# Performance work log

Hardware: AMD Instinct MI355X
Metric: run time of the kernel (lower is better)

Reference implementation:

```python
import jax, jax.numpy as jnp
import numpy as np

N, E, NG, G = 40000, 400000, 64, 512
IN, GP, SP, EP, EA = 4, 3, 3, 6, 4
HID, HEADS, L = 192, 4, 3
DH, FFN = HID // HEADS, 2 * HID


def _ln(x, g, b, eps=1e-5):
    m = x.mean(-1, keepdims=True)
    v = ((x - m) ** 2).mean(-1, keepdims=True)
    return (x - m) * jax.lax.rsqrt(v + eps) * g + b


def _forward(x, edge_attr, group_probs, splitter_probs, endpoint_preds, params,
             edge_index, batch, group_ptr, time_group_ids):
    (W_in, b_in, Wq, Wk, Wv, We, Wo, bo, ln1_g, ln1_b,
     W_ff1, b_ff1, W_ff2, b_ff2, ln2_g, ln2_b,
     W_e1, b_e1, W_e2, b_e2, W_e3, b_e3) = params
    n = x.shape[0]
    src, dst = edge_index[0], edge_index[1]
    # expand per-group predictions to per-node via group ids
    gids = jnp.clip(group_ptr[batch] + time_group_ids, 0, group_probs.shape[0] - 1)
    feat = jnp.concatenate([x, group_probs[gids], splitter_probs, endpoint_preds[gids]], axis=1)
    h = feat @ W_in + b_in  # [N, HID]
    scale = np.float32(1.0 / np.sqrt(DH))
    for l in range(L):  # graph transformer blocks (attention restricted to edges)
        q = (h @ Wq[l]).reshape(n, HEADS, DH)
        k = (h @ Wk[l]).reshape(n, HEADS, DH)
        v = (h @ Wv[l]).reshape(n, HEADS, DH)
        e = (edge_attr @ We[l]).reshape(-1, HEADS, DH)  # [E, H, DH]
        ke = k[src] + e
        ve = v[src] + e
        logit = jnp.einsum('ehd,ehd->eh', q[dst], ke) * scale  # [E, H]
        m = jax.ops.segment_max(logit, dst, num_segments=n)
        m = jnp.where(jnp.isfinite(m), m, 0.0)  # guard nodes with no incoming edges
        a = jnp.exp(logit - m[dst])
        den = jax.ops.segment_sum(a, dst, num_segments=n)
        a = a / (den[dst] + 1e-16)  # per-destination softmax over incoming edges
        msg = jax.ops.segment_sum(a[:, :, None] * ve, dst, num_segments=n).reshape(n, HID)
        h = _ln(h + msg @ Wo[l] + bo[l], ln1_g[l], ln1_b[l])
        ff = jax.nn.relu(h @ W_ff1[l] + b_ff1[l]) @ W_ff2[l] + b_ff2[l]
        h = _ln(h + ff, ln2_g[l], ln2_b[l])
    # edge head: gather src/dst embeddings + edge_attr, concat, MLP -> per-edge logit
    pair = jnp.concatenate([h[src], h[dst], edge_attr], axis=1)  # [E, 2*HID+EA]
    z = jax.nn.relu(pair @ W_e1 + b_e1)
    z = jax.nn.relu(z @ W_e2 + b_e2)
    return z @ W_e3 + b_e3  # [E, 1]


def setup_inputs() -> dict:
    key = jax.random.key(0)
    ks = list(jax.random.split(key, 32))
    it = iter(ks)

    def g(shape, scale=0.05):
        return jax.random.normal(next(it), shape, jnp.float32) * scale

    inp = {
        'x': jax.random.normal(next(it), (N, IN), jnp.float32),
        'edge_index': jax.random.randint(next(it), (2, E), 0, N),
        'edge_attr': jax.random.normal(next(it), (E, EA), jnp.float32),
        'batch': jnp.sort(jax.random.randint(next(it), (N,), 0, NG)),
        'group_ptr': jnp.arange(NG + 1),
        'time_group_ids': jax.random.randint(next(it), (N,), 0, 8),
        'group_probs': jax.random.normal(next(it), (G, GP), jnp.float32),
        'splitter_probs': jax.random.normal(next(it), (N, SP), jnp.float32),
        'endpoint_preds': jax.random.normal(next(it), (G, EP), jnp.float32),
        'W_in': g((IN + GP + SP + EP, HID)), 'b_in': jnp.zeros((HID,), jnp.float32),
        'Wq': g((L, HID, HID)), 'Wk': g((L, HID, HID)), 'Wv': g((L, HID, HID)),
        'We': g((L, EA, HID)), 'Wo': g((L, HID, HID)), 'bo': jnp.zeros((L, HID), jnp.float32),
        'ln1_g': jnp.ones((L, HID), jnp.float32), 'ln1_b': jnp.zeros((L, HID), jnp.float32),
        'W_ff1': g((L, HID, FFN)), 'b_ff1': jnp.zeros((L, FFN), jnp.float32),
        'W_ff2': g((L, FFN, HID)), 'b_ff2': jnp.zeros((L, HID), jnp.float32),
        'ln2_g': jnp.ones((L, HID), jnp.float32), 'ln2_b': jnp.zeros((L, HID), jnp.float32),
        'W_e1': g((2 * HID + EA, HID)), 'b_e1': jnp.zeros((HID,), jnp.float32),
        'W_e2': g((HID, HID // 2)), 'b_e2': jnp.zeros((HID // 2,), jnp.float32),
        'W_e3': g((HID // 2, 1)), 'b_e3': jnp.zeros((1,), jnp.float32),
    }
    return inp


def reference(x, edge_index, edge_attr, batch, group_ptr, time_group_ids,
              group_probs, splitter_probs, endpoint_preds,
              W_in, b_in, Wq, Wk, Wv, We, Wo, bo, ln1_g, ln1_b,
              W_ff1, b_ff1, W_ff2, b_ff2, ln2_g, ln2_b,
              W_e1, b_e1, W_e2, b_e2, W_e3, b_e3):
    params = (W_in, b_in, Wq, Wk, Wv, We, Wo, bo, ln1_g, ln1_b,
              W_ff1, b_ff1, W_ff2, b_ff2, ln2_g, ln2_b,
              W_e1, b_e1, W_e2, b_e2, W_e3, b_e3)
    return _forward(x, edge_attr, group_probs, splitter_probs, endpoint_preds, params,
                    edge_index, batch, group_ptr, time_group_ids)
```

## Files before the change

### kernel.cpp

```cpp
#include <hip/hip_runtime.h>
#include <hip/hip_bf16.h>
#include <math.h>

#define N_NODES 40000
#define N_EDGES 400000
#define GCLIP 511

using short8  = __attribute__((ext_vector_type(8))) short;
using ushort8 = __attribute__((ext_vector_type(8))) unsigned short;
using floatx4 = __attribute__((ext_vector_type(4))) float;

__device__ __forceinline__ void split_bf16(float v, unsigned short& hi, unsigned short& lo) {
    __hip_bfloat16 h = __float2bfloat16(v);
    float r = v - __bfloat162float(h);
    __hip_bfloat16 l = __float2bfloat16(r);
    hi = *(unsigned short*)&h;
    lo = *(unsigned short*)&l;
}
__device__ __forceinline__ unsigned short f2bf(float f) {
    __hip_bfloat16 h = __float2bfloat16(f);
    return *(unsigned short*)&h;
}
__device__ __forceinline__ float bf2f(unsigned short u) {
    __hip_bfloat16 h = *(__hip_bfloat16*)&u;
    return __bfloat162float(h);
}
__device__ __forceinline__ floatx4 mfma16(short8 a, short8 b, floatx4 c) {
    return __builtin_amdgcn_mfma_f32_16x16x32_bf16(a, b, c, 0, 0, 0);
}

__global__ void count_kernel(const int* __restrict__ dst, int* __restrict__ cnt, int E) {
    int e = blockIdx.x * 256 + threadIdx.x;
    if (e < E) atomicAdd(&cnt[dst[e]], 1);
}

__global__ void scan1_kernel(const int* __restrict__ cnt, int* __restrict__ rowp,
                             int* __restrict__ bsum, int n) {
    __shared__ int wsum[16];
    __shared__ int woff[16];
    int tid = threadIdx.x, wave = tid >> 6, lane = tid & 63;
    int i = blockIdx.x * 1024 + tid;
    int v = (i < n) ? cnt[i] : 0;
    int x = v;
    for (int off = 1; off < 64; off <<= 1) {
        int t = __shfl_up(x, off);
        if (lane >= off) x += t;
    }
    if (lane == 63) wsum[wave] = x;
    __syncthreads();
    if (wave == 0 && lane < 16) {
        int s = wsum[lane];
        for (int off = 1; off < 16; off <<= 1) {
            int t = __shfl_up(s, off);
            if (lane >= off) s += t;
        }
        woff[lane] = s;
    }
    __syncthreads();
    int incl = x + ((wave == 0) ? 0 : woff[wave - 1]);
    if (i < n) rowp[i] = incl - v;
    if (tid == 1023) bsum[blockIdx.x] = incl;
}

__global__ void scan2_kernel(const int* __restrict__ bsum, int* __restrict__ boffs,
                             int* __restrict__ rowp, int nb, int n) {
    int lane = threadIdx.x;
    int v = (lane < nb) ? bsum[lane] : 0;
    int x = v;
    for (int off = 1; off < 64; off <<= 1) {
        int t = __shfl_up(x, off);
        if (lane >= off) x += t;
    }
    if (lane < nb) boffs[lane] = x - v;
    if (lane == nb - 1) rowp[n] = x;
}

__global__ void scan3_kernel(int* __restrict__ rowp, int* __restrict__ curs,
                             const int* __restrict__ boffs, int n) {
    int i = blockIdx.x * 1024 + threadIdx.x;
    if (i < n) {
        int v = rowp[i] + boffs[blockIdx.x];
        rowp[i] = v;
        curs[i] = v;
    }
}

__global__ void scatter_kernel(const int* __restrict__ src, const int* __restrict__ dst,
                               int* __restrict__ cursor, int2* __restrict__ csr2, int E) {
    int e = blockIdx.x * 256 + threadIdx.x;
    if (e < E) {
        int pos = atomicAdd(&cursor[dst[e]], 1);
        csr2[pos] = make_int2(src[e], e);
    }
}

__global__ void feat_kernel(const float* __restrict__ x, const int* __restrict__ batch,
                            const int* __restrict__ gptr, const int* __restrict__ tgid,
                            const float* __restrict__ gp, const float* __restrict__ sp,
                            const float* __restrict__ ep,
                            unsigned short* __restrict__ fhi, unsigned short* __restrict__ flo,
                            int n) {
    int idx = blockIdx.x * 256 + threadIdx.x;
    if (idx >= n * 32) return;
    int node = idx >> 5, c = idx & 31;
    float v = 0.f;
    if (c < 4) {
        v = x[node * 4 + c];
    } else if (c < 7) {
        int gid = gptr[batch[node]] + tgid[node];
        gid = min(max(gid, 0), GCLIP);
        v = gp[gid * 3 + (c - 4)];
    } else if (c < 10) {
        v = sp[node * 3 + (c - 7)];
    } else if (c < 16) {
        int gid = gptr[batch[node]] + tgid[node];
        gid = min(max(gid, 0), GCLIP);
        v = ep[gid * 6 + (c - 10)];
    }
    unsigned short hi, lo;
    split_bf16(v, hi, lo);
    fhi[idx] = hi;
    flo[idx] = lo;
}

#define WOFF_WIN 0
#define WOFF_QKV 6144
#define WOFF_WO  337920
#define WOFF_WF1 448512
#define WOFF_WF2 669696
#define WOFF_HSD 890880
#define WOFF_WE2 964608
#define WTOT     983040

__global__ void prep_kernel(const float* __restrict__ W_in, const float* __restrict__ Wq,
                            const float* __restrict__ Wk, const float* __restrict__ Wv,
                            const float* __restrict__ Wo, const float* __restrict__ Wf1,
                            const float* __restrict__ Wf2, const float* __restrict__ We1,
                            const float* __restrict__ We2, unsigned short* __restrict__ wb) {
    int idx = blockIdx.x * 256 + threadIdx.x;
    if (idx >= WTOT) return;
    float val;
    if (idx < WOFF_QKV) {
        int n = idx / 32, k = idx % 32;
        val = (k < 16) ? W_in[k * 192 + n] : 0.f;
    } else if (idx < WOFF_WO) {
        int r = idx - WOFF_QKV; int l = r / 110592; r %= 110592;
        int n = r / 192, k = r % 192;
        const float* s = (n < 192) ? Wq : (n < 384 ? Wk : Wv);
        val = s[l * 36864 + k * 192 + (n % 192)];
        if (n < 192) val *= 0.14433756729740643f;
    } else if (idx < WOFF_WF1) {
        int r = idx - WOFF_WO; int l = r / 36864; r %= 36864;
        int n = r / 192, k = r % 192;
        val = Wo[l * 36864 + k * 192 + n];
    } else if (idx < WOFF_WF2) {
        int r = idx - WOFF_WF1; int l = r / 73728; r %= 73728;
        int n = r / 192, k = r % 192;
        val = Wf1[l * 73728 + k * 384 + n];
    } else if (idx < WOFF_HSD) {
        int r = idx - WOFF_WF2; int l = r / 73728; r %= 73728;
        int n = r / 384, k = r % 384;
        val = Wf2[l * 73728 + k * 192 + n];
    } else if (idx < WOFF_WE2) {
        int r = idx - WOFF_HSD;
        int n = r / 192, k = r % 192;
        val = (n < 192) ? We1[k * 192 + n] : We1[(192 + k) * 192 + (n - 192)];
    } else {
        int r = idx - WOFF_WE2;
        int n = r / 192, k = r % 192;
        val = We2[k * 96 + n];
    }
    wb[idx] = f2bf(val);
}


template <int EPI, int DUAL, int BN, int KCH, int TERMS, int MT>
__global__ __launch_bounds__(256, 4)
void mfma_gemm(const unsigned short* __restrict__ Ahi, const unsigned short* __restrict__ Alo,
               int M, int Ka,
               const unsigned short* __restrict__ B, const float* __restrict__ bias,
               const unsigned short* __restrict__ Rhi, const unsigned short* __restrict__ Rlo,
               const float* __restrict__ lng, const float* __restrict__ lnb,
               unsigned short* __restrict__ Chi, unsigned short* __restrict__ Clo, int ldc) {
    constexpr int NT = BN / 16;
    constexpr int JB = KCH / 8;
    constexpr int SBLK = ((JB + 7) / 8) * 8;
    __shared__ __align__(16) unsigned short sB[BN * SBLK * 8];
    const int tid = threadIdx.x;
    const int wave = tid >> 6, lane = tid & 63;
    const int quad = lane >> 4, l16 = lane & 15;
    const int rbase = blockIdx.x * 64 * MT;
    const int cbase = blockIdx.y * BN;

    floatx4 acc[MT][NT];
#pragma unroll
    for (int mt = 0; mt < MT; ++mt)
#pragma unroll
        for (int nt = 0; nt < NT; ++nt) acc[mt][nt] = (floatx4)0.0f;

    const unsigned short* pah[MT];
    const unsigned short* pal[MT];
#pragma unroll
    for (int mt = 0; mt < MT; ++mt) {
        int r = min(rbase + wave * 16 * MT + mt * 16 + l16, M - 1);
        pah[mt] = Ahi + (size_t)r * Ka + quad * 8;
        pal[mt] = Alo + (size_t)r * Ka + quad * 8;
    }

    for (int kb = 0; kb < Ka; kb += KCH) {
        if (kb) __syncthreads();
        for (int i = tid; i < BN * JB; i += 256) {
            int n = i % BN, j = i / BN;
            *(uint4*)&sB[(n * SBLK + (j ^ (n & 7))) * 8] =
                *(const uint4*)(B + (size_t)(cbase + n) * Ka + kb + j * 8);
        }
        __syncthreads();
        short8 ch[MT], cl[MT];
#pragma unroll
        for (int mt = 0; mt < MT; ++mt) {
            ch[mt] = *(const short8*)(pah[mt] + kb);
            if (TERMS == 2) cl[mt] = *(const short8*)(pal[mt] + kb);
        }
#pragma unroll
        for (int kc = 0; kc < KCH; kc += 32) {
            short8 nh[MT], nl[MT];
#pragma unroll
            for (int mt = 0; mt < MT; ++mt) { nh[mt] = ch[mt]; nl[mt] = ch[mt]; }
            if (kc + 32 < KCH) {
#pragma unroll
                for (int mt = 0; mt < MT; ++mt) {
                    nh[mt] = *(const short8*)(pah[mt] + kb + kc + 32);
                    if (TERMS == 2) nl[mt] = *(const short8*)(pal[mt] + kb + kc + 32);
                }
            }
            const int jbase = kc / 8;
#pragma unroll
            for (int nt = 0; nt < NT; ++nt) {
                int jj = (jbase + quad) ^ (l16 & 7);
                short8 b = *(const short8*)&sB[((nt * 16 + l16) * SBLK + jj) * 8];
#pragma unroll
                for (int mt = 0; mt < MT; ++mt) {
                    acc[mt][nt] = mfma16(ch[mt], b, acc[mt][nt]);
                    if (TERMS == 2) acc[mt][nt] = mfma16(cl[mt], b, acc[mt][nt]);
                }
            }
#pragma unroll
            for (int mt = 0; mt < MT; ++mt) {
                ch[mt] = nh[mt];
                if (TERMS == 2) cl[mt] = nl[mt];
            }
        }
    }

    float bb[NT], gg[NT], be[NT];
#pragma unroll
    for (int nt = 0; nt < NT; ++nt) {
        int colg = cbase + nt * 16 + l16;
        bb[nt] = bias ? bias[colg] : 0.f;
        if (EPI == 2) { gg[nt] = lng[colg]; be[nt] = lnb[colg]; }
    }
#pragma unroll
    for (int mt = 0; mt < MT; ++mt) {
#pragma unroll
        for (int reg = 0; reg < 4; ++reg) {
            int row = rbase + wave * 16 * MT + mt * 16 + quad * 4 + reg;
            if (EPI == 2) {
                int rr = min(row, M - 1);
                float v[NT], s = 0.f, q = 0.f;
#pragma unroll
                for (int nt = 0; nt < NT; ++nt) {
                    size_t off = (size_t)rr * 192 + nt * 16 + l16;
                    float resid = bf2f(Rhi[off]);
                    if (DUAL) resid += bf2f(Rlo[off]);
                    v[nt] = acc[mt][nt][reg] + bb[nt] + resid;
                    s += v[nt]; q += v[nt] * v[nt];
                }
#pragma unroll
                for (int off = 1; off < 16; off <<= 1) {
                    s += __shfl_xor(s, off);
                    q += __shfl_xor(q, off);
                }
                float mean = s * (1.f / 192.f);
                float var = q * (1.f / 192.f) - mean * mean;
                float rs = rsqrtf(var + 1e-5f);
                if (row < M) {
#pragma unroll
                    for (int nt = 0; nt < NT; ++nt) {
                        float r = (v[nt] - mean) * rs * gg[nt] + be[nt];
                        size_t off = (size_t)row * 192 + nt * 16 + l16;
                        if (DUAL) {
                            unsigned short hi, lo;
                            split_bf16(r, hi, lo);
                            Chi[off] = hi; Clo[off] = lo;
                        } else {
                            Chi[off] = f2bf(r);
                        }
                    }
                }
            } else if (row < M) {
#pragma unroll
                for (int nt = 0; nt < NT; ++nt) {
                    float v = acc[mt][nt][reg] + bb[nt];
                    if (EPI == 1) v = fmaxf(v, 0.f);
                    size_t off = (size_t)row * ldc + cbase + nt * 16 + l16;
                    if (DUAL) {
                        unsigned short hi, lo;
                        split_bf16(v, hi, lo);
                        Chi[off] = hi; Clo[off] = lo;
                    } else {
                        Chi[off] = f2bf(v);
                    }
                }
            }
        }
    }
}

template <int EPI, int DUAL, int BN, int NTILES, int TERMS, int KF, int OUTMODE, int MT>
__global__ __launch_bounds__(256, 4)
void mfma_gemm_astat(const unsigned short* __restrict__ Ahi, const unsigned short* __restrict__ Alo,
                     int M, const unsigned short* __restrict__ B, const float* __restrict__ bias,
                     unsigned short* __restrict__ Chi, unsigned short* __restrict__ Clo, int ldc) {
    constexpr int NT = BN / 16;
    constexpr int Ka = KF * 32;
    constexpr int SBLK = KF * 4;
    __shared__ __align__(16) unsigned short sB[BN * SBLK * 8];
    const int tid = threadIdx.x;
    const int wave = tid >> 6, lane = tid & 63;
    const int quad = lane >> 4, l16 = lane & 15;
    const int rbase = blockIdx.x * 64 * MT;

    short8 afh[MT][KF], afl[MT][KF];
#pragma unroll
    for (int mt = 0; mt < MT; ++mt) {
        int r = min(rbase + wave * 16 * MT + mt * 16 + l16, M - 1);
        const unsigned short* ph = Ahi + (size_t)r * Ka + quad * 8;
        const unsigned short* pl = Alo + (size_t)r * Ka + quad * 8;
#pragma unroll
        for (int kf = 0; kf < KF; ++kf) {
            afh[mt][kf] = *(const short8*)(ph + kf * 32);
            if (TERMS == 2) afl[mt][kf] = *(const short8*)(pl + kf * 32);
        }
    }

    for (int t = 0; t < NTILES; ++t) {
        const int cbase = t * BN;
        if (t) __syncthreads();
        for (int i = tid; i < BN * KF * 4; i += 256) {
            int n = i % BN, j = i / BN;
            *(uint4*)&sB[(n * SBLK + (j ^ (n & 7))) * 8] =
                *(const uint4*)(B + (size_t)(cbase + n) * Ka + j * 8);
        }
        __syncthreads();

        floatx4 acc[MT][NT];
#pragma unroll
        for (int mt = 0; mt < MT; ++mt)
#pragma unroll
            for (int nt = 0; nt < NT; ++nt) acc[mt][nt] = (floatx4)0.0f;

#pragma unroll
        for (int kf = 0; kf < KF; ++kf) {
#pragma unroll
            for (int nt = 0; nt < NT; ++nt) {
                int jj = (kf * 4 + quad) ^ (l16 & 7);
                short8 b = *(const short8*)&sB[((nt * 16 + l16) * SBLK + jj) * 8];
#pragma unroll
                for (int mt = 0; mt < MT; ++mt) {
                    acc[mt][nt] = mfma16(afh[mt][kf], b, acc[mt][nt]);
                    if (TERMS == 2) acc[mt][nt] = mfma16(afl[mt][kf], b, acc[mt][nt]);
                }
            }
        }

        float bb[NT];
#pragma unroll
        for (int nt = 0; nt < NT; ++nt) bb[nt] = bias ? bias[cbase + nt * 16 + l16] : 0.f;
#pragma unroll
        for (int mt = 0; mt < MT; ++mt) {
#pragma unroll
            for (int reg = 0; reg < 4; ++reg) {
                int row = rbase + wave * 16 * MT + mt * 16 + quad * 4 + reg;
                if (row < M) {
#pragma unroll
                    for (int nt = 0; nt < NT; ++nt) {
                        float v = acc[mt][nt][reg] + bb[nt];
                        if (EPI == 1) v = fmaxf(v, 0.f);
                        if (OUTMODE == 1) {
                            int c = cbase + nt * 16 + l16;
                            if (c < 192) {
                                Chi[(size_t)row * 192 + c] = f2bf(v);
                            } else {
                                int cc = c - 192;
                                int idx = (cc < 192) ? (cc * 2) : ((cc - 192) * 2 + 1);
                                Clo[(size_t)row * 384 + idx] = f2bf(v);
                            }
                        } else {
                            size_t off = (size_t)row * ldc + cbase + nt * 16 + l16;
                            if (DUAL) {
                                unsigned short hi, lo;
                                split_bf16(v, hi, lo);
                                Chi[off] = hi; Clo[off] = lo;
                            } else {
                                Chi[off] = f2bf(v);
                            }
                        }
                    }
                }
            }
        }
    }
}

__global__ __launch_bounds__(256)
void attn_kernel(const unsigned short* __restrict__ qB, const unsigned short* __restrict__ kvB,
                 const float* __restrict__ ea, const float* __restrict__ We_l,
                 const int2* __restrict__ csr2, const int* __restrict__ row_ptr,
                 unsigned short* __restrict__ msg_hi) {
    __shared__ float sWe[768];
    const int tid = threadIdx.x;
    for (int i = tid; i < 768; i += 256) sWe[i] = We_l[i];
    __syncthreads();

    const int lane = tid & 63;
    const int node = blockIdx.x * 4 + (tid >> 6);
    const int d0 = (lane >> 4) * 48 + (lane & 15) * 3;

    float W[4][3];
#pragma unroll
    for (int w = 0; w < 4; ++w) {
        W[w][0] = sWe[w * 192 + d0];
        W[w][1] = sWe[w * 192 + d0 + 1];
        W[w][2] = sWe[w * 192 + d0 + 2];
    }
    size_t qoff = (size_t)node * 192 + d0;
    float q0 = bf2f(qB[qoff]), q1 = bf2f(qB[qoff + 1]), q2 = bf2f(qB[qoff + 2]);
    float qe0 = q0 * W[0][0] + q1 * W[0][1] + q2 * W[0][2];
    float qe1 = q0 * W[1][0] + q1 * W[1][1] + q2 * W[1][2];
    float qe2 = q0 * W[2][0] + q1 * W[2][1] + q2 * W[2][2];
    float qe3 = q0 * W[3][0] + q1 * W[3][1] + q2 * W[3][2];
#pragma unroll
    for (int off = 1; off < 16; off <<= 1) {
        qe0 += __shfl_xor(qe0, off);
        qe1 += __shfl_xor(qe1, off);
        qe2 += __shfl_xor(qe2, off);
        qe3 += __shfl_xor(qe3, off);
    }

    const unsigned int* kv = (const unsigned int*)kvB;
    const float4* ea4 = (const float4*)ea;

    float den = 0.f;
    float v0 = 0.f, v1 = 0.f, v2 = 0.f;
    float wa0 = 0.f, wa1 = 0.f, wa2 = 0.f, wa3 = 0.f;
    const int beg = row_ptr[node], end = row_ptr[node + 1];
    int p = beg;
    for (; p + 3 < end; p += 4) {
        int2 seA = csr2[p], seB = csr2[p + 1], seC = csr2[p + 2], seD = csr2[p + 3];
        size_t bA = (size_t)seA.x * 192 + d0;
        size_t bB = (size_t)seB.x * 192 + d0;
        size_t bC = (size_t)seC.x * 192 + d0;
        size_t bD = (size_t)seD.x * 192 + d0;
        unsigned int uA0 = kv[bA], uA1 = kv[bA + 1], uA2 = kv[bA + 2];
        unsigned int uB0 = kv[bB], uB1 = kv[bB + 1], uB2 = kv[bB + 2];
        unsigned int uC0 = kv[bC], uC1 = kv[bC + 1], uC2 = kv[bC + 2];
        unsigned int uD0 = kv[bD], uD1 = kv[bD + 1], uD2 = kv[bD + 2];
        float4 wA = ea4[seA.y], wB = ea4[seB.y], wC = ea4[seC.y], wD = ea4[seD.y];
        float dA = q0 * bf2f((unsigned short)uA0) + q1 * bf2f((unsigned short)uA1) + q2 * bf2f((unsigned short)uA2);
        float dB = q0 * bf2f((unsigned short)uB0) + q1 * bf2f((unsigned short)uB1) + q2 * bf2f((unsigned short)uB2);
        float dC = q0 * bf2f((unsigned short)uC0) + q1 * bf2f((unsigned short)uC1) + q2 * bf2f((unsigned short)uC2);
        float dD = q0 * bf2f((unsigned short)uD0) + q1 * bf2f((unsigned short)uD1) + q2 * bf2f((unsigned short)uD2);
#pragma unroll
        for (int off = 1; off < 16; off <<= 1) {
            dA += __shfl_xor(dA, off);
            dB += __shfl_xor(dB, off);
            dC += __shfl_xor(dC, off);
            dD += __shfl_xor(dD, off);
        }
        float pA = __expf(dA + wA.x * qe0 + wA.y * qe1 + wA.z * qe2 + wA.w * qe3);
        float pB = __expf(dB + wB.x * qe0 + wB.y * qe1 + wB.z * qe2 + wB.w * qe3);
        float pC = __expf(dC + wC.x * qe0 + wC.y * qe1 + wC.z * qe2 + wC.w * qe3);
        float pD = __expf(dD + wD.x * qe0 + wD.y * qe1 + wD.z * qe2 + wD.w * qe3);
        den += pA + pB + pC + pD;
        v0 += pA * bf2f((unsigned short)(uA0 >> 16)) + pB * bf2f((unsigned short)(uB0 >> 16))
            + pC * bf2f((unsigned short)(uC0 >> 16)) + pD * bf2f((unsigned short)(uD0 >> 16));
        v1 += pA * bf2f((unsigned short)(uA1 >> 16)) + pB * bf2f((unsigned short)(uB1 >> 16))
            + pC * bf2f((unsigned short)(uC1 >> 16)) + pD * bf2f((unsigned short)(uD1 >> 16));
        v2 += pA * bf2f((unsigned short)(uA2 >> 16)) + pB * bf2f((unsigned short)(uB2 >> 16))
            + pC * bf2f((unsigned short)(uC2 >> 16)) + pD * bf2f((unsigned short)(uD2 >> 16));
        wa0 += pA * wA.x + pB * wB.x + pC * wC.x + pD * wD.x;
        wa1 += pA * wA.y + pB * wB.y + pC * wC.y + pD * wD.y;
        wa2 += pA * wA.z + pB * wB.z + pC * wC.z + pD * wD.z;
        wa3 += pA * wA.w + pB * wB.w + pC * wC.w + pD * wD.w;
    }
    for (; p < end; ++p) {
        int2 se = csr2[p];
        size_t b = (size_t)se.x * 192 + d0;
        unsigned int u0 = kv[b], u1 = kv[b + 1], u2 = kv[b + 2];
        float4 w = ea4[se.y];
        float d = q0 * bf2f((unsigned short)u0) + q1 * bf2f((unsigned short)u1)
                + q2 * bf2f((unsigned short)u2);
#pragma unroll
        for (int off = 1; off < 16; off <<= 1) d += __shfl_xor(d, off);
        float pe = __expf(d + w.x * qe0 + w.y * qe1 + w.z * qe2 + w.w * qe3);
        den += pe;
        v0 += pe * bf2f((unsigned short)(u0 >> 16));
        v1 += pe * bf2f((unsigned short)(u1 >> 16));
        v2 += pe * bf2f((unsigned short)(u2 >> 16));
        wa0 += pe * w.x;
        wa1 += pe * w.y;
        wa2 += pe * w.z;
        wa3 += pe * w.w;
    }
    float inv = 1.f / (den + 1e-16f);
    float m0 = (v0 + wa0 * W[0][0] + wa1 * W[1][0] + wa2 * W[2][0] + wa3 * W[3][0]) * inv;
    float m1 = (v1 + wa0 * W[0][1] + wa1 * W[1][1] + wa2 * W[2][1] + wa3 * W[3][1]) * inv;
    float m2 = (v2 + wa0 * W[0][2] + wa1 * W[1][2] + wa2 * W[2][2] + wa3 * W[3][2]) * inv;
    size_t ob = (size_t)node * 192 + d0;
    msg_hi[ob]     = f2bf(m0);
    msg_hi[ob + 1] = f2bf(m1);
    msg_hi[ob + 2] = f2bf(m2);
}

__global__ __launch_bounds__(256, 2)
void edge_head_kernel(const unsigned short* __restrict__ hsd, const float* __restrict__ ea,
                      const int* __restrict__ src, const int* __restrict__ dst,
                      const float* __restrict__ W1e, const float* __restrict__ b1,
                      const unsigned short* __restrict__ W2hi,
                      const float* __restrict__ b2, const float* __restrict__ W3,
                      const float* __restrict__ b3, float* __restrict__ out) {
    __shared__ __align__(16) unsigned short sW[96 * 192];
    __shared__ __align__(16) float sWe1[768];
    __shared__ __align__(16) float sB1[192];
    const int tid = threadIdx.x;
    const int wave = tid >> 6, lane = tid & 63;
    const int quad = lane >> 4, l16 = lane & 15;
    const int ebase = blockIdx.x * 128;

    for (int i = tid; i < 768; i += 256) sWe1[i] = W1e[i];
    if (tid < 192) sB1[tid] = b1[tid];
    for (int i = tid; i < 96 * 24; i += 256) {
        int n = i % 96, j = i / 96;
        *(uint4*)&sW[(n * 24 + (j ^ (n & 7))) * 8] = *(const uint4*)(W2hi + (size_t)n * 192 + j * 8);
    }

    const int e0 = ebase + wave * 32 + l16;
    const int e1 = e0 + 16;
    const int s0 = src[e0], d0n = dst[e0];
    const int s1 = src[e1], d1n = dst[e1];
    const float4 eav0 = *(const float4*)(ea + (size_t)e0 * 4);
    const float4 eav1 = *(const float4*)(ea + (size_t)e1 * 4);
    const unsigned short* hs0_p = hsd + (size_t)s0 * 384 + quad * 8;
    const unsigned short* hd0_p = hsd + (size_t)d0n * 384 + 192 + quad * 8;
    const unsigned short* hs1_p = hsd + (size_t)s1 * 384 + quad * 8;
    const unsigned short* hd1_p = hsd + (size_t)d1n * 384 + 192 + quad * 8;

    floatx4 acc[2][6];
#pragma unroll
    for (int g = 0; g < 2; ++g)
#pragma unroll
        for (int nt = 0; nt < 6; ++nt) acc[g][nt] = (floatx4)0.0f;
    __syncthreads();

    ushort8 hs0_c = *(const ushort8*)hs0_p;
    ushort8 hd0_c = *(const ushort8*)hd0_p;
    ushort8 hs1_c = *(const ushort8*)hs1_p;
    ushort8 hd1_c = *(const ushort8*)hd1_p;
#pragma unroll
    for (int kc = 0; kc < 192; kc += 32) {
        ushort8 hs0_n = hs0_c, hd0_n = hd0_c, hs1_n = hs1_c, hd1_n = hd1_c;
        if (kc + 32 < 192) {
            hs0_n = *(const ushort8*)(hs0_p + kc + 32);
            hd0_n = *(const ushort8*)(hd0_p + kc + 32);
            hs1_n = *(const ushort8*)(hs1_p + kc + 32);
            hd1_n = *(const ushort8*)(hd1_p + kc + 32);
        }
        const int c0 = kc + quad * 8;
        float wb1[8], w0v[8], w1v[8], w2v[8], w3v[8];
        *(float4*)&wb1[0] = *(const float4*)&sB1[c0];
        *(float4*)&wb1[4] = *(const float4*)&sB1[c0 + 4];
        *(float4*)&w0v[0] = *(const float4*)&sWe1[c0];
        *(float4*)&w0v[4] = *(const float4*)&sWe1[c0 + 4];
        *(float4*)&w1v[0] = *(const float4*)&sWe1[192 + c0];
        *(float4*)&w1v[4] = *(const float4*)&sWe1[192 + c0 + 4];
        *(float4*)&w2v[0] = *(const float4*)&sWe1[384 + c0];
        *(float4*)&w2v[4] = *(const float4*)&sWe1[384 + c0 + 4];
        *(float4*)&w3v[0] = *(const float4*)&sWe1[576 + c0];
        *(float4*)&w3v[4] = *(const float4*)&sWe1[576 + c0 + 4];
        ushort8 ah0, ah1;
#pragma unroll
        for (int j = 0; j < 8; ++j) {
            float base = wb1[j];
            float ce0 = base + eav0.x * w0v[j] + eav0.y * w1v[j]
                      + eav0.z * w2v[j] + eav0.w * w3v[j];
            float ce1 = base + eav1.x * w0v[j] + eav1.y * w1v[j]
                      + eav1.z * w2v[j] + eav1.w * w3v[j];
            ah0[j] = f2bf(fmaxf(bf2f(hs0_c[j]) + bf2f(hd0_c[j]) + ce0, 0.f));
            ah1[j] = f2bf(fmaxf(bf2f(hs1_c[j]) + bf2f(hd1_c[j]) + ce1, 0.f));
        }
        short8 a0 = *(short8*)&ah0, a1 = *(short8*)&ah1;
        const int jbase = kc / 8;
#pragma unroll
        for (int nt = 0; nt < 6; ++nt) {
            int jj = (jbase + quad) ^ (l16 & 7);
            short8 bh = *(const short8*)&sW[((nt * 16 + l16) * 24 + jj) * 8];
            acc[0][nt] = mfma16(a0, bh, acc[0][nt]);
            acc[1][nt] = mfma16(a1, bh, acc[1][nt]);
        }
        hs0_c = hs0_n; hd0_c = hd0_n; hs1_c = hs1_n; hd1_c = hd1_n;
    }

    float w3[6], bb2[6];
#pragma unroll
    for (int nt = 0; nt < 6; ++nt) {
        int col = nt * 16 + l16;
        w3[nt] = W3[col];
        bb2[nt] = b2[col];
    }
    float b3v = b3[0];
#pragma unroll
    for (int g = 0; g < 2; ++g) {
#pragma unroll
        for (int reg = 0; reg < 4; ++reg) {
            float sacc = 0.f;
#pragma unroll
            for (int nt = 0; nt < 6; ++nt) {
                float z = fmaxf(acc[g][nt][reg] + bb2[nt], 0.f);
                sacc = fmaf(z, w3[nt], sacc);
            }
#pragma unroll
            for (int off = 1; off < 16; off <<= 1) sacc += __shfl_xor(sacc, off);
            if (l16 == 0) out[ebase + wave * 32 + g * 16 + quad * 4 + reg] = sacc + b3v;
        }
    }
}

extern "C" void kernel_launch(void* const* d_in, const int* in_sizes, int n_in,
                              void* d_out, int out_size, void* d_ws, size_t ws_size,
                              hipStream_t stream) {
    const float* x     = (const float*)d_in[0];
    const int*   eidx  = (const int*)d_in[1];
    const float* ea    = (const float*)d_in[2];
    const int*   batch = (const int*)d_in[3];
    const int*   gptr  = (const int*)d_in[4];
    const int*   tgid  = (const int*)d_in[5];
    const float* gp    = (const float*)d_in[6];
    const float* sp    = (const float*)d_in[7];
    const float* epp   = (const float*)d_in[8];
    const float* W_in  = (const float*)d_in[9];
    const float* b_in  = (const float*)d_in[10];
    const float* Wq    = (const float*)d_in[11];
    const float* Wk    = (const float*)d_in[12];
    const float* Wv    = (const float*)d_in[13];
    const float* We    = (const float*)d_in[14];
    const float* Wo    = (const float*)d_in[15];
    const float* bo    = (const float*)d_in[16];
    const float* ln1g  = (const float*)d_in[17];
    const float* ln1b  = (const float*)d_in[18];
    const float* Wf1   = (const float*)d_in[19];
    const float* bf1   = (const float*)d_in[20];
    const float* Wf2   = (const float*)d_in[21];
    const float* bf2   = (const float*)d_in[22];
    const float* ln2g  = (const float*)d_in[23];
    const float* ln2b  = (const float*)d_in[24];
    const float* We1   = (const float*)d_in[25];
    const float* be1   = (const float*)d_in[26];
    const float* We2   = (const float*)d_in[27];
    const float* be2   = (const float*)d_in[28];
    const float* We3   = (const float*)d_in[29];
    const float* be3   = (const float*)d_in[30];
    const int* src = eidx;
    const int* dst = eidx + N_EDGES;

    unsigned short* ub = (unsigned short*)d_ws;
    unsigned short* featH = ub;
    unsigned short* featL = ub + 1280000;
    unsigned short* hH    = ub + 2560000;
    unsigned short* hL    = ub + 10240000;
    unsigned short* htH   = ub + 17920000;
    unsigned short* htL   = ub + 25600000;
    unsigned short* msgH  = ub + 33280000;
    unsigned short* rbuf  = ub + 48640000;
    unsigned short* qB    = rbuf;
    unsigned short* kvB   = rbuf + 7680000;
    unsigned short* ffH   = rbuf;
    unsigned short* hsdB  = rbuf;
    unsigned short* wb    = ub + 79360000;
    int* ib   = (int*)(ub + 80343040);
    int* cnt  = ib;
    int* rowp = ib + 40000;
    int* curs = ib + 80004;
    int2* csr2 = (int2*)(ib + 120004);
    int* bsum  = ib + 920004;
    int* boffs = ib + 920044;

    hipMemsetAsync(cnt, 0, N_NODES * sizeof(int), stream);
    count_kernel<<<1563, 256, 0, stream>>>(dst, cnt, N_EDGES);
    scan1_kernel<<<40, 1024, 0, stream>>>(cnt, rowp, bsum, N_NODES);
    scan2_kernel<<<1, 64, 0, stream>>>(bsum, boffs, rowp, 40, N_NODES);
    scan3_kernel<<<40, 1024, 0, stream>>>(rowp, curs, boffs, N_NODES);
    scatter_kernel<<<1563, 256, 0, stream>>>(src, dst, curs, csr2, N_EDGES);
    feat_kernel<<<5000, 256, 0, stream>>>(x, batch, gptr, tgid, gp, sp, epp, featH, featL, N_NODES);
    prep_kernel<<<3840, 256, 0, stream>>>(W_in, Wq, Wk, Wv, Wo, Wf1, Wf2, We1, We2, wb);

    dim3 blk(256);
    mfma_gemm<0, 1, 192, 32, 2, 1><<<dim3(625, 1), blk, 0, stream>>>(featH, featL, N_NODES, 32,
        wb + WOFF_WIN, b_in, nullptr, nullptr, nullptr, nullptr, hH, hL, 192);

    for (int l = 0; l < 3; ++l) {
        const unsigned short* wq = wb + WOFF_QKV + l * 110592;
        mfma_gemm_astat<0, 0, 96, 6, 1, 6, 1, 1><<<625, blk, 0, stream>>>(hH, hH, N_NODES,
            wq, nullptr, qB, kvB, 0);
        attn_kernel<<<10000, blk, 0, stream>>>(qB, kvB, ea, We + l * 768, csr2, rowp, msgH);
        mfma_gemm<2, 1, 192, 64, 1, 1><<<dim3(625, 1), blk, 0, stream>>>(msgH, msgH, N_NODES, 192,
            wb + WOFF_WO + l * 36864, bo + l * 192, hH, hL, ln1g + l * 192, ln1b + l * 192,
            htH, htL, 192);
        mfma_gemm_astat<1, 0, 96, 4, 1, 6, 0, 1><<<625, blk, 0, stream>>>(htH, htH, N_NODES,
            wb + WOFF_WF1 + l * 73728, bf1 + l * 384, ffH, nullptr, 384);
        mfma_gemm<2, 1, 192, 64, 1, 1><<<dim3(625, 1), blk, 0, stream>>>(ffH, ffH, N_NODES, 384,
            wb + WOFF_WF2 + l * 73728, bf2 + l * 192, htH, htL, ln2g + l * 192, ln2b + l * 192,
            hH, hL, 192);
    }

    mfma_gemm_astat<0, 0, 96, 4, 1, 6, 0, 1><<<625, blk, 0, stream>>>(hH, hH, N_NODES,
        wb + WOFF_HSD, nullptr, hsdB, nullptr, 384);
    edge_head_kernel<<<3125, blk, 0, stream>>>(hsdB, ea, src, dst,
        We1 + 384 * 192, be1, wb + WOFF_WE2, be2, We3, be3, (float*)d_out);
}
```

Before: 811.4 us.

## Process edge head in destination-sorted CSR order and raise occupancy hint

The edge head now walks edges in CSR (destination-sorted) order, with the scatter kernel also recording each slot's destination. Gathers of destination embeddings then hit the same rows for consecutive lanes, which should improve cache locality. Outputs are written back through the stored original edge id, turning coalesced stores into scattered ones, and ea reads become indirect. Launch bounds are raised to 3 blocks per SM, which risks register spills.

```diff
diff --git a/kernel.cpp b/kernel.cpp
--- a/kernel.cpp
+++ b/kernel.cpp
@@ -86,11 +86,14 @@
 }
 
 __global__ void scatter_kernel(const int* __restrict__ src, const int* __restrict__ dst,
-                               int* __restrict__ cursor, int2* __restrict__ csr2, int E) {
+                               int* __restrict__ cursor, int2* __restrict__ csr2,
+                               int* __restrict__ csrd, int E) {
     int e = blockIdx.x * 256 + threadIdx.x;
     if (e < E) {
-        int pos = atomicAdd(&cursor[dst[e]], 1);
+        int d = dst[e];
+        int pos = atomicAdd(&cursor[d], 1);
         csr2[pos] = make_int2(src[e], e);
+        csrd[pos] = d;
     }
 }
 
@@ -522,9 +525,9 @@
     msg_hi[ob + 2] = f2bf(m2);
 }
 
-__global__ __launch_bounds__(256, 2)
+__global__ __launch_bounds__(256, 3)
 void edge_head_kernel(const unsigned short* __restrict__ hsd, const float* __restrict__ ea,
-                      const int* __restrict__ src, const int* __restrict__ dst,
+                      const int2* __restrict__ csr2, const int* __restrict__ csrd,
                       const float* __restrict__ W1e, const float* __restrict__ b1,
                       const unsigned short* __restrict__ W2hi,
                       const float* __restrict__ b2, const float* __restrict__ W3,
@@ -535,7 +538,7 @@
     const int tid = threadIdx.x;
     const int wave = tid >> 6, lane = tid & 63;
     const int quad = lane >> 4, l16 = lane & 15;
-    const int ebase = blockIdx.x * 128;
+    const int pbase = blockIdx.x * 128;
 
     for (int i = tid; i < 768; i += 256) sWe1[i] = W1e[i];
     if (tid < 192) sB1[tid] = b1[tid];
@@ -544,12 +547,13 @@
         *(uint4*)&sW[(n * 24 + (j ^ (n & 7))) * 8] = *(const uint4*)(W2hi + (size_t)n * 192 + j * 8);
     }
 
-    const int e0 = ebase + wave * 32 + l16;
-    const int e1 = e0 + 16;
-    const int s0 = src[e0], d0n = dst[e0];
-    const int s1 = src[e1], d1n = dst[e1];
-    const float4 eav0 = *(const float4*)(ea + (size_t)e0 * 4);
-    const float4 eav1 = *(const float4*)(ea + (size_t)e1 * 4);
+    const int p0 = pbase + wave * 32 + l16;
+    const int p1 = p0 + 16;
+    const int2 se0 = csr2[p0], se1 = csr2[p1];
+    const int d0n = csrd[p0], d1n = csrd[p1];
+    const int s0 = se0.x, s1 = se1.x;
+    const float4 eav0 = *(const float4*)(ea + (size_t)se0.y * 4);
+    const float4 eav1 = *(const float4*)(ea + (size_t)se1.y * 4);
     const unsigned short* hs0_p = hsd + (size_t)s0 * 384 + quad * 8;
     const unsigned short* hd0_p = hsd + (size_t)d0n * 384 + 192 + quad * 8;
     const unsigned short* hs1_p = hsd + (size_t)s1 * 384 + quad * 8;
@@ -630,7 +634,10 @@
             }
 #pragma unroll
             for (int off = 1; off < 16; off <<= 1) sacc += __shfl_xor(sacc, off);
-            if (l16 == 0) out[ebase + wave * 32 + g * 16 + quad * 4 + reg] = sacc + b3v;
+            if (l16 == 0) {
+                int slot = pbase + wave * 32 + g * 16 + quad * 4 + reg;
+                out[csr2[slot].y] = sacc + b3v;
+            }
         }
     }
 }
@@ -693,13 +700,14 @@
     int2* csr2 = (int2*)(ib + 120004);
     int* bsum  = ib + 920004;
     int* boffs = ib + 920044;
+    int* csrd  = ib + 920084;
 
     hipMemsetAsync(cnt, 0, N_NODES * sizeof(int), stream);
     count_kernel<<<1563, 256, 0, stream>>>(dst, cnt, N_EDGES);
     scan1_kernel<<<40, 1024, 0, stream>>>(cnt, rowp, bsum, N_NODES);
     scan2_kernel<<<1, 64, 0, stream>>>(bsum, boffs, rowp, 40, N_NODES);
     scan3_kernel<<<40, 1024, 0, stream>>>(rowp, curs, boffs, N_NODES);
-    scatter_kernel<<<1563, 256, 0, stream>>>(src, dst, curs, csr2, N_EDGES);
+    scatter_kernel<<<1563, 256, 0, stream>>>(src, dst, curs, csr2, csrd, N_EDGES);
     feat_kernel<<<5000, 256, 0, stream>>>(x, batch, gptr, tgid, gp, sp, epp, featH, featL, N_NODES);
     prep_kernel<<<3840, 256, 0, stream>>>(W_in, Wq, Wk, Wv, Wo, Wf1, Wf2, We1, We2, wb);
 
@@ -724,6 +732,6 @@
 
     mfma_gemm_astat<0, 0, 96, 4, 1, 6, 0, 1><<<625, blk, 0, stream>>>(hH, hH, N_NODES,
         wb + WOFF_HSD, nullptr, hsdB, nullptr, 384);
-    edge_head_kernel<<<3125, blk, 0, stream>>>(hsdB, ea, src, dst,
+    edge_head_kernel<<<3125, blk, 0, stream>>>(hsdB, ea, csr2, csrd,
         We1 + 384 * 192, be1, wb + WOFF_WE2, be2, We3, be3, (float*)d_out);
 }
```

Result: no change. 817.5 us (+0.7%).
